# Optimization experiments

Hardware: AMD Instinct MI355X
Metric: run time of the kernel (lower is better)

## Reference

```python
import jax, jax.numpy as jnp
import numpy as np

C_S = 128
C_T = 128
C_OUT = 128


def _proj(x, W, b):
    # 1x1x1 Conv3d == per-voxel linear over channel dim. x: [B, Cin, T, H, W]
    return jnp.einsum('oc,bcthw->bothw', W, x) + b[None, :, None, None, None]


def setup_inputs() -> dict:
    key = jax.random.key(0)
    ks = jax.random.split(key, 12)
    B, T, H, W = 4, 4, 32, 32
    spatial_features = jax.random.normal(ks[0], (B, T, C_S, H, W), dtype=jnp.float32)
    temporal_features = jax.random.normal(ks[1], (B, C_T, T, H, W), dtype=jnp.float32)
    def w(k, o, i):
        return jax.random.normal(k, (o, i), dtype=jnp.float32) * (i ** -0.5)
    return {
        'spatial_features': spatial_features,
        'temporal_features': temporal_features,
        'Wq': w(ks[2], C_OUT, C_S), 'bq': jnp.zeros((C_OUT,), jnp.float32),
        'Wk': w(ks[3], C_OUT, C_T), 'bk': jnp.zeros((C_OUT,), jnp.float32),
        'Wv': w(ks[4], C_OUT, C_T), 'bv': jnp.zeros((C_OUT,), jnp.float32),
        'Wo': w(ks[5], C_OUT, C_OUT), 'bo': jnp.zeros((C_OUT,), jnp.float32),
    }


def reference(spatial_features, temporal_features, Wq, bq, Wk, bk, Wv, bv, Wo, bo):
    B, T, C_s, H, W = spatial_features.shape
    N = T * H * W
    scale = C_OUT ** -0.5
    # permute(0,2,1,3,4): [B, T, C_s, H, W] -> [B, C_s, T, H, W]
    x_s = jnp.transpose(spatial_features, (0, 2, 1, 3, 4))
    q = _proj(x_s, Wq, bq)                 # [B, C_out, T, H, W]
    k = _proj(temporal_features, Wk, bk)   # [B, C_out, T, H, W]
    v = _proj(temporal_features, Wv, bv)   # [B, C_out, T, H, W]
    Q = q.reshape(B, C_OUT, N).transpose(0, 2, 1)  # [B, N, C]
    K = k.reshape(B, C_OUT, N)                     # [B, C, N]
    V = v.reshape(B, C_OUT, N).transpose(0, 2, 1)  # [B, N, C]
    attn = jax.nn.softmax(jnp.einsum('bnc,bcm->bnm', Q, K) * scale, axis=2)  # [B, N, N]
    out = jnp.einsum('bnm,bmc->bnc', attn, V)      # [B, N, C]
    out = out.transpose(0, 2, 1).reshape(B, C_OUT, T, H, W)
    return _proj(out, Wo, bo)
```

## Files before the change

### kernel.cpp

```cpp
#include <hip/hip_runtime.h>
#include <cstddef>

#define NDIM 4096
#define SCALE 0.08838834764831843f
#define SOFT_BIAS 8.0f
#define SCALE_L2E 0.12751741843533886f
#define BIAS_L2E  11.541560327111707f

typedef _Float16 h8 __attribute__((ext_vector_type(8)));
typedef _Float16 h4 __attribute__((ext_vector_type(4)));
typedef _Float16 h2 __attribute__((ext_vector_type(2)));
typedef float    f4 __attribute__((ext_vector_type(4)));

__device__ __forceinline__ h8 cvt_w_frag(const float* wp) {
    const float4 u0 = *(const float4*)wp;
    const float4 u1 = *(const float4*)(wp + 4);
    h8 f;
    f[0]=(_Float16)u0.x; f[1]=(_Float16)u0.y; f[2]=(_Float16)u0.z; f[3]=(_Float16)u0.w;
    f[4]=(_Float16)u1.x; f[5]=(_Float16)u1.y; f[6]=(_Float16)u1.z; f[7]=(_Float16)u1.w;
    return f;
}

__global__ __launch_bounds__(256) void prep_w_kernel(
    const float* __restrict__ Wq, const float* __restrict__ Wk,
    const float* __restrict__ Wv, const float* __restrict__ Wo,
    _Float16* __restrict__ Whf)
{
    const int gid = blockIdx.x * 256 + threadIdx.x;
    const int mat = gid >> 11, rem = gid & 2047;
    const int ot = rem >> 8, ks = (rem >> 6) & 3, l = rem & 63;
    const float* src = mat == 0 ? Wq : mat == 1 ? Wk : mat == 2 ? Wv : Wo;
    const h8 f = cvt_w_frag(src + (size_t)(16 * ot + (l & 15)) * 128 + 32 * ks + 8 * (l >> 4));
    *(h8*)(Whf + (size_t)gid * 8) = f;
}

__global__ __launch_bounds__(256, 3) void proj_qkv_kernel(
    const float* __restrict__ spatial, const float* __restrict__ temporal,
    const _Float16* __restrict__ Whf,
    const float* __restrict__ bq, const float* __restrict__ bk,
    const float* __restrict__ bv,
    _Float16* __restrict__ Qh, _Float16* __restrict__ Kh, _Float16* __restrict__ Vt)
{
    __shared__ __align__(16) _Float16 Xl[32 * 136];
    const int tid = threadIdx.x;
    const int n0  = blockIdx.x * 32;
    const int b   = blockIdx.y;
    const int p   = blockIdx.z;
    const float* __restrict__ bias = (p == 0) ? bq : (p == 1) ? bk : bv;

    {
        const float* src; size_t rs;
        if (p == 0) { const int t = n0 >> 10, hw0 = n0 & 1023;
            src = spatial + (((size_t)(b * 4 + t) * 128) << 10) + hw0; rs = 1024; }
        else { src = temporal + ((size_t)(b * 128) << 12) + n0; rs = 4096; }
        #pragma unroll
        for (int i = 0; i < 2; ++i) {
            const int ii = tid + 256 * i;
            const int c2 = ii >> 3, j = ii & 7;
            const float4 v0 = *(const float4*)(src + (size_t)(2 * c2) * rs + 4 * j);
            const float4 v1 = *(const float4*)(src + (size_t)(2 * c2 + 1) * rs + 4 * j);
            const float a0[4] = {v0.x, v0.y, v0.z, v0.w};
            const float a1[4] = {v1.x, v1.y, v1.z, v1.w};
            #pragma unroll
            for (int u = 0; u < 4; ++u) {
                h2 pk; pk[0] = (_Float16)a0[u]; pk[1] = (_Float16)a1[u];
                *(h2*)&Xl[(4 * j + u) * 136 + 2 * c2] = pk;
            }
        }
    }
    __syncthreads();

    const int w = tid >> 6, lane = tid & 63, n16 = tid & 15, q4 = (tid >> 4) & 3;

    h8 wf[2][4];
    #pragma unroll
    for (int otl = 0; otl < 2; ++otl)
        #pragma unroll
        for (int ks = 0; ks < 4; ++ks)
            wf[otl][ks] = *(const h8*)(Whf + ((size_t)(((p * 8 + 2 * w + otl) * 4 + ks)) << 9)
                                           + lane * 8);
    h8 xf[2][4];
    #pragma unroll
    for (int ns = 0; ns < 2; ++ns)
        #pragma unroll
        for (int ks = 0; ks < 4; ++ks)
            xf[ns][ks] = *(const h8*)&Xl[(16 * ns + n16) * 136 + 32 * ks + 8 * q4];

    if (p < 2) {
        f4 acc[2][2];
        #pragma unroll
        for (int i = 0; i < 2; ++i) { acc[i][0] = (f4)0.0f; acc[i][1] = (f4)0.0f; }
        #pragma unroll
        for (int otl = 0; otl < 2; ++otl)
            #pragma unroll
            for (int ns = 0; ns < 2; ++ns)
                #pragma unroll
                for (int ks = 0; ks < 4; ++ks)
                    acc[otl][ns] = __builtin_amdgcn_mfma_f32_16x16x32_f16(
                        wf[otl][ks], xf[ns][ks], acc[otl][ns], 0, 0, 0);
        _Float16* __restrict__ dst = (p == 0) ? Qh : Kh;
        #pragma unroll
        for (int otl = 0; otl < 2; ++otl) {
            const float4 bb = *(const float4*)&bias[16 * (2 * w + otl) + 4 * q4];
            #pragma unroll
            for (int ns = 0; ns < 2; ++ns) {
                h4 r;
                r[0]=(_Float16)(acc[otl][ns][0]+bb.x); r[1]=(_Float16)(acc[otl][ns][1]+bb.y);
                r[2]=(_Float16)(acc[otl][ns][2]+bb.z); r[3]=(_Float16)(acc[otl][ns][3]+bb.w);
                *(h4*)(dst + ((size_t)b * NDIM + n0 + 16 * ns + n16) * 128
                           + 16 * (2 * w + otl) + 4 * q4) = r;
            }
        }
    } else {
        f4 acc[2][2];
        #pragma unroll
        for (int i = 0; i < 2; ++i) { acc[i][0] = (f4)0.0f; acc[i][1] = (f4)0.0f; }
        #pragma unroll
        for (int ns = 0; ns < 2; ++ns)
            #pragma unroll
            for (int otl = 0; otl < 2; ++otl)
                #pragma unroll
                for (int ks = 0; ks < 4; ++ks)
                    acc[ns][otl] = __builtin_amdgcn_mfma_f32_16x16x32_f16(
                        xf[ns][ks], wf[otl][ks], acc[ns][otl], 0, 0, 0);
        #pragma unroll
        for (int ns = 0; ns < 2; ++ns)
            #pragma unroll
            for (int otl = 0; otl < 2; ++otl) {
                const float bb = bias[16 * (2 * w + otl) + n16];
                h4 r;
                r[0]=(_Float16)(acc[ns][otl][0]+bb); r[1]=(_Float16)(acc[ns][otl][1]+bb);
                r[2]=(_Float16)(acc[ns][otl][2]+bb); r[3]=(_Float16)(acc[ns][otl][3]+bb);
                *(h4*)(Vt + ((size_t)(b * 128 + 16 * (2 * w + otl) + n16) << 12)
                          + n0 + 16 * ns + 4 * q4) = r;
            }
    }
}

__global__ __launch_bounds__(256, 2) void attn_kernel(
    const _Float16* __restrict__ Qh, const _Float16* __restrict__ Kh,
    const _Float16* __restrict__ Vt, _Float16* __restrict__ Opart,
    float* __restrict__ lpart)
{
    __shared__ __align__(16) _Float16 sh[17408];

    const int tid  = threadIdx.x;
    const int w    = tid >> 6, lane = tid & 63;
    const int g    = w >> 1,  p    = w & 1;
    const int n16  = lane & 15, q4 = lane >> 4;

    const int id = blockIdx.x + 32 * blockIdx.y + 128 * blockIdx.z;
    const int pi = (id & 7) + 8 * (id >> 8);
    const int qt = (id >> 3) & 31;
    const int hf = pi & 3, b = pi >> 2;
    const int n0 = qt * 128;
    const int mb = hf * 1024;

    h8 qf[4][4];
    {
        const _Float16* Qb = Qh + ((size_t)b * NDIM + n0 + 64 * g + n16) * 128;
        #pragma unroll
        for (int qs = 0; qs < 4; ++qs)
            #pragma unroll
            for (int ks = 0; ks < 4; ++ks)
                qf[qs][ks] = *(const h8*)(Qb + (size_t)(16 * qs) * 128 + 32 * ks + 8 * q4);
    }

    const _Float16* kb = Kh + ((size_t)b * NDIM + mb + 16 * p + n16) * 128 + 8 * q4;
    const _Float16* vb = Vt + (((size_t)(b * 128 + 64 * p + n16)) << 12) + mb + 8 * q4;

    h8 kfr[4], vfr[4];
    #pragma unroll
    for (int ks = 0; ks < 4; ++ks)
        kfr[ks] = *(const h8*)(kb + 32 * ks);

    f4 oacc[4][4];
    #pragma unroll
    for (int i = 0; i < 4; ++i)
        #pragma unroll
        for (int j = 0; j < 4; ++j) oacc[i][j] = (f4)0.0f;
    float lsum[4] = {0.0f, 0.0f, 0.0f, 0.0f};

    for (int it = 0; it < 32; ++it) {
        __syncthreads();
        const int cur = it & 1;
        _Float16* __restrict__ Pg = sh + cur * 5120 + g * 2560;
        const _Float16* __restrict__ Pp = sh + (cur ^ 1) * 5120 + g * 2560;

        if (it > 0) {
            h8 pf[4];
            #pragma unroll
            for (int qs = 0; qs < 4; ++qs)
                pf[qs] = *(const h8*)&Pp[(16 * qs + n16) * 40 + 8 * q4];
            #pragma unroll
            for (int qs = 0; qs < 4; ++qs)
                #pragma unroll
                for (int ct = 0; ct < 4; ++ct)
                    oacc[qs][ct] = __builtin_amdgcn_mfma_f32_16x16x32_f16(
                        pf[qs], vfr[ct], oacc[qs][ct], 0, 0, 0);
        }

        {
            const _Float16* vt = vb + 32 * it;
            #pragma unroll
            for (int ct = 0; ct < 4; ++ct)
                vfr[ct] = *(const h8*)(vt + ((size_t)ct << 16));
        }

        f4 sacc[4];
        #pragma unroll
        for (int qs = 0; qs < 4; ++qs) sacc[qs] = (f4)0.0f;
        #pragma unroll
        for (int ks = 0; ks < 4; ++ks) {
            const h8 kf = kfr[ks];
            #pragma unroll
            for (int qs = 0; qs < 4; ++qs)
                sacc[qs] = __builtin_amdgcn_mfma_f32_16x16x32_f16(kf, qf[qs][ks], sacc[qs], 0, 0, 0);
        }

        if (it < 31) {
            kb += 32 * 128;
            #pragma unroll
            for (int ks = 0; ks < 4; ++ks)
                kfr[ks] = *(const h8*)(kb + 32 * ks);
        }

        #pragma unroll
        for (int qs = 0; qs < 4; ++qs) {
            h4 pk;
            #pragma unroll
            for (int r = 0; r < 4; ++r) {
                const float e = __builtin_amdgcn_exp2f(fmaf(sacc[qs][r], SCALE_L2E, -BIAS_L2E));
                lsum[qs] += e;
                pk[r] = (_Float16)e;
            }
            *(h4*)&Pg[(16 * qs + n16) * 40 + 16 * p + 4 * q4] = pk;
        }
    }

    __syncthreads();
    {
        const _Float16* __restrict__ Pp = sh + 5120 + g * 2560;
        h8 pf[4];
        #pragma unroll
        for (int qs = 0; qs < 4; ++qs)
            pf[qs] = *(const h8*)&Pp[(16 * qs + n16) * 40 + 8 * q4];
        #pragma unroll
        for (int qs = 0; qs < 4; ++qs)
            #pragma unroll
            for (int ct = 0; ct < 4; ++ct)
                oacc[qs][ct] = __builtin_amdgcn_mfma_f32_16x16x32_f16(
                    pf[qs], vfr[ct], oacc[qs][ct], 0, 0, 0);
    }

    #pragma unroll
    for (int qs = 0; qs < 4; ++qs) {
        lsum[qs] += __shfl_xor(lsum[qs], 16, 64);
        lsum[qs] += __shfl_xor(lsum[qs], 32, 64);
    }
    if (q4 == 0) {
        float* lb = lpart + ((size_t)((hf * 2 + p) * 4 + b)) * NDIM + n0 + 64 * g;
        #pragma unroll
        for (int qs = 0; qs < 4; ++qs) lb[16 * qs + n16] = lsum[qs];
    }

    __syncthreads();
    #pragma unroll
    for (int qs = 0; qs < 4; ++qs)
        #pragma unroll
        for (int ct = 0; ct < 4; ++ct)
            #pragma unroll
            for (int r = 0; r < 4; ++r)
                sh[(64 * g + 16 * qs + 4 * q4 + r) * 136 + 64 * p + 16 * ct + n16] =
                    (_Float16)oacc[qs][ct][r];
    __syncthreads();
    const size_t ob = ((size_t)(hf * 4 + b) * NDIM + n0) * 128;
    #pragma unroll
    for (int i = 0; i < 8; ++i) {
        const int ii  = tid + 256 * i;
        const int row = ii >> 4, c8 = (ii & 15) * 8;
        *(int4*)(Opart + ob + (size_t)row * 128 + c8) = *(const int4*)&sh[row * 136 + c8];
    }
}

__global__ __launch_bounds__(256, 2) void proj_final_kernel(
    const _Float16* __restrict__ Opart, const float* __restrict__ lpart,
    const _Float16* __restrict__ Whf, const float* __restrict__ bo,
    float* __restrict__ out)
{
    __shared__ __align__(16) _Float16 Xl[32 * 136];
    __shared__ float lrow[32];
    __shared__ __align__(16) float Ofin[128 * 36];
    const int tid = threadIdx.x;
    const int n0  = blockIdx.x * 32;
    const int b   = blockIdx.y;

    if (tid < 32) {
        float l = 0.0f;
        #pragma unroll
        for (int h8i = 0; h8i < 8; ++h8i)
            l += lpart[((size_t)(h8i * 4 + b)) * NDIM + n0 + tid];
        lrow[tid] = 1.0f / l;
    }
    float vals[2][8];
    int rows[2], c8s[2];
    #pragma unroll
    for (int i = 0; i < 2; ++i) {
        const int ii = tid + 256 * i;
        rows[i] = ii >> 4; c8s[i] = (ii & 15) * 8;
        #pragma unroll
        for (int j = 0; j < 8; ++j) vals[i][j] = 0.0f;
        #pragma unroll
        for (int hf = 0; hf < 4; ++hf) {
            const h8 o = *(const h8*)(Opart + ((size_t)(hf * 4 + b) * NDIM + n0 + rows[i]) * 128
                                      + c8s[i]);
            #pragma unroll
            for (int j = 0; j < 8; ++j) vals[i][j] += (float)o[j];
        }
    }
    __syncthreads();
    #pragma unroll
    for (int i = 0; i < 2; ++i) {
        const float linv = lrow[rows[i]];
        h8 r;
        #pragma unroll
        for (int j = 0; j < 8; ++j) r[j] = (_Float16)(vals[i][j] * linv);
        *(h8*)&Xl[rows[i] * 136 + c8s[i]] = r;
    }
    __syncthreads();

    const int w = tid >> 6, lane = tid & 63, n16 = tid & 15, q4 = (tid >> 4) & 3;

    h8 wf[2][4];
    #pragma unroll
    for (int otl = 0; otl < 2; ++otl)
        #pragma unroll
        for (int ks = 0; ks < 4; ++ks)
            wf[otl][ks] = *(const h8*)(Whf + ((size_t)(((3 * 8 + 2 * w + otl) * 4 + ks)) << 9)
                                           + lane * 8);
    h8 xf[2][4];
    #pragma unroll
    for (int ns = 0; ns < 2; ++ns)
        #pragma unroll
        for (int ks = 0; ks < 4; ++ks)
            xf[ns][ks] = *(const h8*)&Xl[(16 * ns + n16) * 136 + 32 * ks + 8 * q4];

    f4 acc[2][2];
    #pragma unroll
    for (int i = 0; i < 2; ++i) { acc[i][0] = (f4)0.0f; acc[i][1] = (f4)0.0f; }
    #pragma unroll
    for (int otl = 0; otl < 2; ++otl)
        #pragma unroll
        for (int ns = 0; ns < 2; ++ns)
            #pragma unroll
            for (int ks = 0; ks < 4; ++ks)
                acc[otl][ns] = __builtin_amdgcn_mfma_f32_16x16x32_f16(
                    wf[otl][ks], xf[ns][ks], acc[otl][ns], 0, 0, 0);

    #pragma unroll
    for (int otl = 0; otl < 2; ++otl) {
        const float4 bb = *(const float4*)&bo[16 * (2 * w + otl) + 4 * q4];
        const float bias[4] = {bb.x, bb.y, bb.z, bb.w};
        #pragma unroll
        for (int ns = 0; ns < 2; ++ns)
            #pragma unroll
            for (int r = 0; r < 4; ++r)
                Ofin[(16 * (2 * w + otl) + 4 * q4 + r) * 36 + 16 * ns + n16] =
                    acc[otl][ns][r] + bias[r];
    }
    __syncthreads();
    #pragma unroll
    for (int i = 0; i < 4; ++i) {
        const int ii  = tid + 256 * i;
        const int row = ii >> 3, j = ii & 7;
        *(float4*)(out + (((size_t)(b * 128 + row)) << 12) + n0 + 4 * j) =
            *(const float4*)&Ofin[row * 36 + 4 * j];
    }
}

extern "C" void kernel_launch(void* const* d_in, const int* in_sizes, int n_in,
                              void* d_out, int out_size, void* d_ws, size_t ws_size,
                              hipStream_t stream)
{
    const float* spatial  = (const float*)d_in[0];
    const float* temporal = (const float*)d_in[1];
    const float* Wq = (const float*)d_in[2];
    const float* bq = (const float*)d_in[3];
    const float* Wk = (const float*)d_in[4];
    const float* bk = (const float*)d_in[5];
    const float* Wv = (const float*)d_in[6];
    const float* bv = (const float*)d_in[7];
    const float* Wo = (const float*)d_in[8];
    const float* bo = (const float*)d_in[9];

    char* ws = (char*)d_ws;
    _Float16* Qh    = (_Float16*)(ws);
    _Float16* Kh    = (_Float16*)(ws + (4u  << 20));
    _Float16* Vt    = (_Float16*)(ws + (8u  << 20));
    _Float16* Opart = (_Float16*)(ws + (12u << 20));
    float*    lpart = (float*)   (ws + (28u << 20));
    _Float16* Whf   = (_Float16*)(ws + (28u << 20) + (512u << 10));

    prep_w_kernel<<<32, 256, 0, stream>>>(Wq, Wk, Wv, Wo, Whf);
    proj_qkv_kernel<<<dim3(128, 4, 3), 256, 0, stream>>>(
        spatial, temporal, Whf, bq, bk, bv, Qh, Kh, Vt);
    attn_kernel<<<dim3(32, 4, 4), 256, 0, stream>>>(Qh, Kh, Vt, Opart, lpart);
    proj_final_kernel<<<dim3(128, 4), 256, 0, stream>>>(Opart, lpart, Whf, bo,
                                                        (float*)d_out);
}
```

Baseline: 161.8 us.

## Stage K/V tiles through LDS with async global_load_lds and multi-buffering

K and V fragments are no longer loaded from global memory straight into registers by each wave. They are now staged into shared memory with asynchronous global_load_lds copies: K is double-buffered with an XOR swizzle and V is triple-buffered. Each tile is loaded once per block and shared across waves, which removes duplicate global reads. MFMA sections are also bracketed with s_setprio to favour the matrix work. The cost is a larger LDS footprint (about 60KB per block), which may limit occupancy at two blocks per CU, plus extra LDS read traffic.

```diff
diff --git a/kernel.cpp b/kernel.cpp
--- a/kernel.cpp
+++ b/kernel.cpp
@@ -2,8 +2,6 @@
 #include <cstddef>
 
 #define NDIM 4096
-#define SCALE 0.08838834764831843f
-#define SOFT_BIAS 8.0f
 #define SCALE_L2E 0.12751741843533886f
 #define BIAS_L2E  11.541560327111707f
 
@@ -11,6 +9,12 @@
 typedef _Float16 h4 __attribute__((ext_vector_type(4)));
 typedef _Float16 h2 __attribute__((ext_vector_type(2)));
 typedef float    f4 __attribute__((ext_vector_type(4)));
+
+__device__ __forceinline__ void gld_lds16(const void* g, void* l) {
+    __builtin_amdgcn_global_load_lds(
+        (const __attribute__((address_space(1))) void*)g,
+        (__attribute__((address_space(3))) void*)l, 16, 0, 0);
+}
 
 __device__ __forceinline__ h8 cvt_w_frag(const float* wp) {
     const float4 u0 = *(const float4*)wp;
@@ -142,7 +146,7 @@
     const _Float16* __restrict__ Vt, _Float16* __restrict__ Opart,
     float* __restrict__ lpart)
 {
-    __shared__ __align__(16) _Float16 sh[17408];
+    __shared__ __align__(16) _Float16 sh[30720];
 
     const int tid  = threadIdx.x;
     const int w    = tid >> 6, lane = tid & 63;
@@ -156,6 +160,22 @@
     const int n0 = qt * 128;
     const int mb = hf * 1024;
 
+    const int r4 = lane >> 4, c16 = lane & 15;
+    const _Float16* kg0 = Kh + ((size_t)b * NDIM + mb + 8 * w + r4) * 128
+                             + ((c16 * 8) ^ ((r4 & 7) << 3));
+    const _Float16* kg1 = Kh + ((size_t)b * NDIM + mb + 8 * w + 4 + r4) * 128
+                             + ((c16 * 8) ^ (((4 + r4) & 7) << 3));
+    const int vr = lane >> 2, vc4 = lane & 3;
+    const _Float16* vg0 = Vt + (((size_t)(b * 128 + 32 * w + vr)) << 12) + mb + vc4 * 8;
+    const _Float16* vg1 = vg0 + ((size_t)16 << 12);
+
+    const int kd = (8 * w) * 128;
+    const int vd = (32 * w) * 32;
+
+    gld_lds16(kg0, sh + kd);            gld_lds16(kg1, sh + kd + 512);
+    gld_lds16(vg0, sh + 8192 + vd);     gld_lds16(vg1, sh + 8192 + vd + 512);
+    kg0 += 32 * 128; kg1 += 32 * 128; vg0 += 32; vg1 += 32;
+
     h8 qf[4][4];
     {
         const _Float16* Qb = Qh + ((size_t)b * NDIM + n0 + 64 * g + n16) * 128;
@@ -166,63 +186,68 @@
                 qf[qs][ks] = *(const h8*)(Qb + (size_t)(16 * qs) * 128 + 32 * ks + 8 * q4);
     }
 
-    const _Float16* kb = Kh + ((size_t)b * NDIM + mb + 16 * p + n16) * 128 + 8 * q4;
-    const _Float16* vb = Vt + (((size_t)(b * 128 + 64 * p + n16)) << 12) + mb + 8 * q4;
-
-    h8 kfr[4], vfr[4];
-    #pragma unroll
-    for (int ks = 0; ks < 4; ++ks)
-        kfr[ks] = *(const h8*)(kb + 32 * ks);
-
     f4 oacc[4][4];
     #pragma unroll
     for (int i = 0; i < 4; ++i)
         #pragma unroll
         for (int j = 0; j < 4; ++j) oacc[i][j] = (f4)0.0f;
     float lsum[4] = {0.0f, 0.0f, 0.0f, 0.0f};
+
+    const int kx = (n16 & 7) << 3;
+    const int krow = (16 * p + n16) * 128;
 
     for (int it = 0; it < 32; ++it) {
         __syncthreads();
         const int cur = it & 1;
-        _Float16* __restrict__ Pg = sh + cur * 5120 + g * 2560;
-        const _Float16* __restrict__ Pp = sh + (cur ^ 1) * 5120 + g * 2560;
+        _Float16* __restrict__ Pg = sh + 20480 + cur * 5120 + g * 2560;
+        const _Float16* __restrict__ Pp = sh + 20480 + (cur ^ 1) * 5120 + g * 2560;
+
+        if (it < 31) {
+            _Float16* kdst = sh + (cur ^ 1) * 4096 + kd;
+            gld_lds16(kg0, kdst); gld_lds16(kg1, kdst + 512);
+            const int vst = (it + 1) % 3;
+            _Float16* vdst = sh + 8192 + vst * 4096 + vd;
+            gld_lds16(vg0, vdst); gld_lds16(vg1, vdst + 512);
+            kg0 += 32 * 128; kg1 += 32 * 128; vg0 += 32; vg1 += 32;
+        }
 
         if (it > 0) {
-            h8 pf[4];
+            const int vrd = (it - 1) % 3;
+            const _Float16* __restrict__ VP = sh + 8192 + vrd * 4096;
+            h8 pf[4], vf[4];
             #pragma unroll
             for (int qs = 0; qs < 4; ++qs)
                 pf[qs] = *(const h8*)&Pp[(16 * qs + n16) * 40 + 8 * q4];
+            #pragma unroll
+            for (int ct = 0; ct < 4; ++ct)
+                vf[ct] = *(const h8*)&VP[(64 * p + 16 * ct + n16) * 32 + 8 * q4];
+            __builtin_amdgcn_s_setprio(1);
             #pragma unroll
             for (int qs = 0; qs < 4; ++qs)
                 #pragma unroll
                 for (int ct = 0; ct < 4; ++ct)
                     oacc[qs][ct] = __builtin_amdgcn_mfma_f32_16x16x32_f16(
-                        pf[qs], vfr[ct], oacc[qs][ct], 0, 0, 0);
-        }
-
+                        pf[qs], vf[ct], oacc[qs][ct], 0, 0, 0);
+            __builtin_amdgcn_s_setprio(0);
+        }
+
+        f4 sacc[4];
+        #pragma unroll
+        for (int qs = 0; qs < 4; ++qs) sacc[qs] = (f4)0.0f;
         {
-            const _Float16* vt = vb + 32 * it;
-            #pragma unroll
-            for (int ct = 0; ct < 4; ++ct)
-                vfr[ct] = *(const h8*)(vt + ((size_t)ct << 16));
-        }
-
-        f4 sacc[4];
-        #pragma unroll
-        for (int qs = 0; qs < 4; ++qs) sacc[qs] = (f4)0.0f;
-        #pragma unroll
-        for (int ks = 0; ks < 4; ++ks) {
-            const h8 kf = kfr[ks];
-            #pragma unroll
-            for (int qs = 0; qs < 4; ++qs)
-                sacc[qs] = __builtin_amdgcn_mfma_f32_16x16x32_f16(kf, qf[qs][ks], sacc[qs], 0, 0, 0);
-        }
-
-        if (it < 31) {
-            kb += 32 * 128;
+            const _Float16* __restrict__ KB = sh + cur * 4096;
+            h8 kf[4];
             #pragma unroll
             for (int ks = 0; ks < 4; ++ks)
-                kfr[ks] = *(const h8*)(kb + 32 * ks);
+                kf[ks] = *(const h8*)&KB[krow + ((32 * ks + 8 * q4) ^ kx)];
+            __builtin_amdgcn_s_setprio(1);
+            #pragma unroll
+            for (int ks = 0; ks < 4; ++ks)
+                #pragma unroll
+                for (int qs = 0; qs < 4; ++qs)
+                    sacc[qs] = __builtin_amdgcn_mfma_f32_16x16x32_f16(
+                        kf[ks], qf[qs][ks], sacc[qs], 0, 0, 0);
+            __builtin_amdgcn_s_setprio(0);
         }
 
         #pragma unroll
@@ -240,17 +265,21 @@
 
     __syncthreads();
     {
-        const _Float16* __restrict__ Pp = sh + 5120 + g * 2560;
-        h8 pf[4];
+        const _Float16* __restrict__ Pp = sh + 20480 + 5120 + g * 2560;
+        const _Float16* __restrict__ VP = sh + 8192 + 1 * 4096;
+        h8 pf[4], vf[4];
         #pragma unroll
         for (int qs = 0; qs < 4; ++qs)
             pf[qs] = *(const h8*)&Pp[(16 * qs + n16) * 40 + 8 * q4];
         #pragma unroll
+        for (int ct = 0; ct < 4; ++ct)
+            vf[ct] = *(const h8*)&VP[(64 * p + 16 * ct + n16) * 32 + 8 * q4];
+        #pragma unroll
         for (int qs = 0; qs < 4; ++qs)
             #pragma unroll
             for (int ct = 0; ct < 4; ++ct)
                 oacc[qs][ct] = __builtin_amdgcn_mfma_f32_16x16x32_f16(
-                    pf[qs], vfr[ct], oacc[qs][ct], 0, 0, 0);
+                    pf[qs], vf[ct], oacc[qs][ct], 0, 0, 0);
     }
 
     #pragma unroll
```

New measurement: 136.4 us. 1.19x faster.
